# Performance work log

Hardware: AMD Instinct MI355X
Metric: run time of the kernel (lower is better)

Reference implementation:

```python
import jax, jax.numpy as jnp
import numpy as np

L, H, E, V = 8, 16, 1024, 32000   # n_layer, n_head, n_embd, vocab_size
B, T = 4, 1024                      # batch, block_size
HS = E // H                         # head_size = 64


def _ln(x, g, b, eps=1e-5):
    m = jnp.mean(x, axis=-1, keepdims=True)
    v = jnp.mean((x - m) ** 2, axis=-1, keepdims=True)
    return (x - m) / jnp.sqrt(v + eps) * g + b


def setup_inputs() -> dict:
    key = jax.random.key(0)
    ks = jax.random.split(key, 21)
    s = 0.02
    n = lambda k, shp: (jax.random.normal(k, shp, dtype=jnp.float32) * s)
    return {
        'idx': jax.random.randint(ks[0], (B, T), 0, V),
        'tok_emb': n(ks[1], (V, E)),
        'pos_emb': n(ks[2], (T, E)),
        'ln1_g': jnp.ones((L, E), jnp.float32),
        'ln1_b': jnp.zeros((L, E), jnp.float32),
        'Wq': n(ks[3], (L, E, E)),
        'Wk': n(ks[4], (L, E, E)),
        'Wv': n(ks[5], (L, E, E)),
        'Wo': n(ks[6], (L, E, E)),
        'bo': jnp.zeros((L, E), jnp.float32),
        'ln2_g': jnp.ones((L, E), jnp.float32),
        'ln2_b': jnp.zeros((L, E), jnp.float32),
        'W1': n(ks[7], (L, E, 4 * E)),
        'b1': jnp.zeros((L, 4 * E), jnp.float32),
        'W2': n(ks[8], (L, 4 * E, E)),
        'b2': jnp.zeros((L, E), jnp.float32),
        'lnf_g': jnp.ones((E,), jnp.float32),
        'lnf_b': jnp.zeros((E,), jnp.float32),
        'Wlm': n(ks[9], (E, V)),
        'blm': jnp.zeros((V,), jnp.float32),
    }


def reference(idx, tok_emb, pos_emb, ln1_g, ln1_b, Wq, Wk, Wv, Wo, bo,
              ln2_g, ln2_b, W1, b1, W2, b2, lnf_g, lnf_b, Wlm, blm):
    x = tok_emb[idx] + pos_emb[:T]               # [B, T, E]
    scale = E ** -0.5                            # NOTE: source scales by C=n_embd, not head_size
    mask = jnp.tril(jnp.ones((T, T), dtype=bool))
    for l in range(L):
        h = _ln(x, ln1_g[l], ln1_b[l])
        q = (h @ Wq[l]).reshape(B, T, H, HS).transpose(0, 2, 1, 3)   # [B,H,T,hs]
        k = (h @ Wk[l]).reshape(B, T, H, HS).transpose(0, 2, 1, 3)
        v = (h @ Wv[l]).reshape(B, T, H, HS).transpose(0, 2, 1, 3)
        att = jnp.einsum('bhqd,bhkd->bhqk', q, k) * scale
        att = jnp.where(mask, att, -jnp.inf)
        att = jax.nn.softmax(att, axis=-1)
        o = jnp.einsum('bhqk,bhkd->bhqd', att, v)
        o = o.transpose(0, 2, 1, 3).reshape(B, T, E)                 # concat heads
        x = x + o @ Wo[l] + bo[l]
        h2 = _ln(x, ln2_g[l], ln2_b[l])
        x = x + jax.nn.relu(h2 @ W1[l] + b1[l]) @ W2[l] + b2[l]
    x = _ln(x, lnf_g, lnf_b)
    return x @ Wlm + blm                          # logits [B, T, V]
```

## Files before the change

kernel.cpp:

```cpp
#include <hip/hip_runtime.h>
#include <math.h>

#define L_ 8
#define H_ 16
#define E_ 1024
#define V_ 32000
#define B_ 4
#define T_ 1024
#define HS_ 64
#define M_ 4096
#define QKVS_ 3072

typedef __attribute__((ext_vector_type(8))) short short8;
typedef __attribute__((ext_vector_type(4))) float f32x4;

__device__ __forceinline__ unsigned short f2bf(float f) {
  unsigned int u = __builtin_bit_cast(unsigned int, f);
  u += 0x7fffu + ((u >> 16) & 1u);
  return (unsigned short)(u >> 16);
}

__global__ __launch_bounds__(256) void k_embed(
    const int* __restrict__ idx, const float* __restrict__ tok,
    const float* __restrict__ pos, float* __restrict__ x) {
  int bt = blockIdx.x;
  int t  = bt & (T_ - 1);
  int token = idx[bt];
  const float4* te = (const float4*)(tok + (size_t)token * E_);
  const float4* pe = (const float4*)(pos + (size_t)t * E_);
  float4* xo = (float4*)(x + (size_t)bt * E_);
  int i = threadIdx.x;
  float4 a = te[i], b = pe[i];
  xo[i] = make_float4(a.x + b.x, a.y + b.y, a.z + b.z, a.w + b.w);
}

__global__ __launch_bounds__(256) void k_wt(
    const float* __restrict__ W, unsigned short* __restrict__ WT,
    int K, int N, size_t ss, size_t ds) {
  __shared__ unsigned short t[64][66];
  const float* Ws = W + (size_t)blockIdx.z * ss;
  unsigned short* Wd = WT + (size_t)blockIdx.z * ds;
  int n0 = blockIdx.x * 64, k0 = blockIdx.y * 64;
  int tid = threadIdx.x;
  int c = tid & 63, r4 = tid >> 6;
  #pragma unroll
  for (int i = 0; i < 16; ++i) {
    int kr = i * 4 + r4;
    t[kr][c] = f2bf(Ws[(size_t)(k0 + kr) * N + n0 + c]);
  }
  __syncthreads();
  #pragma unroll
  for (int i = 0; i < 16; ++i) {
    int nr = i * 4 + r4;
    Wd[(size_t)(n0 + nr) * K + k0 + c] = t[c][nr];
  }
}

__device__ __forceinline__ float blk_sum256(float v, float* red) {
  #pragma unroll
  for (int o = 1; o < 64; o <<= 1) v += __shfl_xor(v, o);
  int wid = threadIdx.x >> 6, lane = threadIdx.x & 63;
  if (lane == 0) red[wid] = v;
  __syncthreads();
  v = red[0] + red[1] + red[2] + red[3];
  __syncthreads();
  return v;
}

__global__ __launch_bounds__(256) void k_ln_bf(
    const float* __restrict__ X, const float* __restrict__ g,
    const float* __restrict__ b, unsigned short* __restrict__ Y) {
  __shared__ float red[4];
  int row = blockIdx.x;
  int i = threadIdx.x;
  float4 xv = ((const float4*)(X + (size_t)row * E_))[i];
  float s = xv.x + xv.y + xv.z + xv.w;
  s = blk_sum256(s, red);
  float mean = s * (1.0f / E_);
  float dx = xv.x - mean, dy = xv.y - mean, dz = xv.z - mean, dw = xv.w - mean;
  float vs = dx*dx + dy*dy + dz*dz + dw*dw;
  vs = blk_sum256(vs, red);
  float rstd = rsqrtf(vs * (1.0f / E_) + 1e-5f);
  float4 gv = ((const float4*)g)[i];
  float4 bv = ((const float4*)b)[i];
  ushort4 o;
  o.x = f2bf(dx * rstd * gv.x + bv.x);
  o.y = f2bf(dy * rstd * gv.y + bv.y);
  o.z = f2bf(dz * rstd * gv.z + bv.z);
  o.w = f2bf(dw * rstd * gv.w + bv.w);
  ((ushort4*)(Y + (size_t)row * E_))[i] = o;
}

template<int BN, int OT, bool RELU, bool RES>
__global__ __launch_bounds__(256) void k_gemm_tn(
    const unsigned short* __restrict__ A, const unsigned short* __restrict__ BT,
    const float* __restrict__ bias, const float* __restrict__ R,
    void* __restrict__ Cout, int M, int N, int K) {
  constexpr int NF = BN / 32;
  __shared__ __attribute__((aligned(16))) unsigned short As[128 * 64];
  __shared__ __attribute__((aligned(16))) unsigned short Bs[BN * 64];
  int tid = threadIdx.x;
  int lane = tid & 63, w = tid >> 6;
  int lr = lane & 15, lq = lane >> 4;
  int m0 = blockIdx.x * 128, n0 = blockIdx.y * BN;
  int wr = (w >> 1) * 64, wc = (w & 1) * (BN / 2);

  int srow = w * 8 + (lane >> 3);
  int skoff = ((lane & 7) ^ (lane >> 3)) * 8;
  const unsigned short* a0 = A + (size_t)(m0 + srow) * K + skoff;
  const unsigned short* b0 = BT + (size_t)(n0 + srow) * K + skoff;

  f32x4 acc[4][NF] = {};

  for (int k0 = 0; k0 < K; k0 += 64) {
    __syncthreads();
    #pragma unroll
    for (int j = 0; j < 4; ++j)
      __builtin_amdgcn_global_load_lds(
          (const __attribute__((address_space(1))) void*)(a0 + (size_t)(j * 32) * K + k0),
          (__attribute__((address_space(3))) void*)(As + j * 2048 + w * 512), 16, 0, 0);
    #pragma unroll
    for (int j = 0; j < NF; ++j)
      __builtin_amdgcn_global_load_lds(
          (const __attribute__((address_space(1))) void*)(b0 + (size_t)(j * 32) * K + k0),
          (__attribute__((address_space(3))) void*)(Bs + j * 2048 + w * 512), 16, 0, 0);
    __syncthreads();
    short8 af[4][2], bf[NF][2];
    #pragma unroll
    for (int m = 0; m < 4; ++m)
      #pragma unroll
      for (int ks = 0; ks < 2; ++ks)
        af[m][ks] = *(const short8*)&As[(wr + m * 16 + lr) * 64 + (((ks * 4 + lq) ^ (lr & 7)) << 3)];
    #pragma unroll
    for (int n = 0; n < NF; ++n)
      #pragma unroll
      for (int ks = 0; ks < 2; ++ks)
        bf[n][ks] = *(const short8*)&Bs[(wc + n * 16 + lr) * 64 + (((ks * 4 + lq) ^ (lr & 7)) << 3)];
    #pragma unroll
    for (int ks = 0; ks < 2; ++ks)
      #pragma unroll
      for (int m = 0; m < 4; ++m)
        #pragma unroll
        for (int n = 0; n < NF; ++n)
          acc[m][n] = __builtin_amdgcn_mfma_f32_16x16x32_bf16(af[m][ks], bf[n][ks], acc[m][n], 0, 0, 0);
  }

  #pragma unroll
  for (int m = 0; m < 4; ++m) {
    #pragma unroll
    for (int n = 0; n < NF; ++n) {
      int col = n0 + wc + n * 16 + lr;
      float bv = bias ? bias[col] : 0.0f;
      #pragma unroll
      for (int i = 0; i < 4; ++i) {
        size_t row = (size_t)(m0 + wr + m * 16 + lq * 4 + i);
        float v = acc[m][n][i] + bv;
        if (RELU) v = fmaxf(v, 0.0f);
        if (RES)  v += R[row * N + col];
        if (OT == 0) ((float*)Cout)[row * N + col] = v;
        else ((unsigned short*)Cout)[row * N + col] = f2bf(v);
      }
    }
  }
}

template<int OT, bool RELU, bool RES>
__global__ __launch_bounds__(256) void k_gemm_bf(
    const unsigned short* __restrict__ A, const float* __restrict__ W,
    const float* __restrict__ bias, const float* __restrict__ R,
    void* __restrict__ Cout, int M, int N, int K) {
  __shared__ unsigned short As[128][40];
  __shared__ unsigned short Bs[128][40];
  int tid = threadIdx.x;
  int lane = tid & 63, wid = tid >> 6;
  int m0 = blockIdx.x * 128, n0 = blockIdx.y * 128;
  int wr = (wid >> 1) * 64, wc = (wid & 1) * 64;
  f32x4 acc[4][4] = {};
  int a_row = tid >> 1, a_koff = (tid & 1) * 16;
  int b_nb = tid & 31, b_kb = (tid >> 5) * 4;
  int lr = lane & 15, lq = lane >> 4;
  for (int k0 = 0; k0 < K; k0 += 32) {
    const unsigned short* ap = A + (size_t)(m0 + a_row) * K + k0 + a_koff;
    uint4 av0 = *(const uint4*)ap;
    uint4 av1 = *(const uint4*)(ap + 8);
    float wv[4][4];
    #pragma unroll
    for (int dk = 0; dk < 4; ++dk) {
      const float* wrow = W + (size_t)(k0 + b_kb + dk) * N + n0 + b_nb;
      #pragma unroll
      for (int j = 0; j < 4; ++j) wv[j][dk] = wrow[32 * j];
    }
    __syncthreads();
    *(uint4*)&As[a_row][a_koff]     = av0;
    *(uint4*)&As[a_row][a_koff + 8] = av1;
    #pragma unroll
    for (int j = 0; j < 4; ++j) {
      ushort4 pk;
      pk.x = f2bf(wv[j][0]); pk.y = f2bf(wv[j][1]);
      pk.z = f2bf(wv[j][2]); pk.w = f2bf(wv[j][3]);
      *(ushort4*)&Bs[b_nb + 32 * j][b_kb] = pk;
    }
    __syncthreads();
    short8 af[4], bf[4];
    #pragma unroll
    for (int m = 0; m < 4; ++m) af[m] = *(const short8*)&As[wr + m * 16 + lr][lq * 8];
    #pragma unroll
    for (int n = 0; n < 4; ++n) bf[n] = *(const short8*)&Bs[wc + n * 16 + lr][lq * 8];
    #pragma unroll
    for (int m = 0; m < 4; ++m)
      #pragma unroll
      for (int n = 0; n < 4; ++n)
        acc[m][n] = __builtin_amdgcn_mfma_f32_16x16x32_bf16(af[m], bf[n], acc[m][n], 0, 0, 0);
  }
  #pragma unroll
  for (int m = 0; m < 4; ++m) {
    #pragma unroll
    for (int n = 0; n < 4; ++n) {
      int col = n0 + wc + n * 16 + lr;
      float bv = bias ? bias[col] : 0.0f;
      #pragma unroll
      for (int i = 0; i < 4; ++i) {
        size_t row = (size_t)(m0 + wr + m * 16 + lq * 4 + i);
        float v = acc[m][n][i] + bv;
        if (RELU) v = fmaxf(v, 0.0f);
        if (RES)  v += R[row * N + col];
        if (OT == 0) ((float*)Cout)[row * N + col] = v;
        else ((unsigned short*)Cout)[row * N + col] = f2bf(v);
      }
    }
  }
}

__global__ __launch_bounds__(256) void k_fattn(
    const unsigned short* __restrict__ QKV, unsigned short* __restrict__ O) {
  __shared__ unsigned short Ks[64][72];
  __shared__ unsigned short Vs[64][74];
  __shared__ unsigned short Pl[4][32][72];
  int tid = threadIdx.x;
  int lane = tid & 63, wid = tid >> 6;
  int lr = lane & 15, lq = lane >> 4;
  int qt = blockIdx.x, bh = blockIdx.y;
  int b = bh >> 4, h = bh & 15;
  size_t base = ((size_t)b * T_) * QKVS_ + h * HS_;
  int q0w = qt * 128 + wid * 32;

  short8 qf[2][2];
  #pragma unroll
  for (int g = 0; g < 2; ++g)
    #pragma unroll
    for (int s = 0; s < 2; ++s)
      qf[g][s] = *(const short8*)(QKV + base + (size_t)(q0w + g * 16 + lr) * QKVS_ + s * 32 + lq * 8);

  f32x4 o_acc[2][4] = {};
  float mrun[2][4], lrun[2][4];
  #pragma unroll
  for (int g = 0; g < 2; ++g)
    #pragma unroll
    for (int i = 0; i < 4; ++i) { mrun[g][i] = -1e30f; lrun[g][i] = 0.0f; }
  const float sc = 0.03125f * 1.44269504f;
  int r = tid >> 2, cc = (tid & 3) * 16;
  int ntiles = 2 * qt + 2;

  for (int t = 0; t < ntiles; ++t) {
    __syncthreads();
    const unsigned short* kp = QKV + base + 1024 + (size_t)(t * 64 + r) * QKVS_ + cc;
    const unsigned short* vp = kp + 1024;
    uint4 k0v = *(const uint4*)kp, k1v = *(const uint4*)(kp + 8);
    uint4 v0v = *(const uint4*)vp, v1v = *(const uint4*)(vp + 8);
    *(uint4*)&Ks[r][cc] = k0v;
    *(uint4*)&Ks[r][cc + 8] = k1v;
    unsigned short vt[16];
    *(uint4*)&vt[0] = v0v; *(uint4*)&vt[8] = v1v;
    #pragma unroll
    for (int j = 0; j < 16; ++j) Vs[cc + j][r] = vt[j];
    __syncthreads();

    f32x4 sa[2][4] = {};
    #pragma unroll
    for (int nt = 0; nt < 4; ++nt)
      #pragma unroll
      for (int s = 0; s < 2; ++s) {
        short8 kf = *(const short8*)&Ks[nt * 16 + lr][s * 32 + lq * 8];
        sa[0][nt] = __builtin_amdgcn_mfma_f32_16x16x32_bf16(qf[0][s], kf, sa[0][nt], 0, 0, 0);
        sa[1][nt] = __builtin_amdgcn_mfma_f32_16x16x32_bf16(qf[1][s], kf, sa[1][nt], 0, 0, 0);
      }

    bool diag = (t >= 2 * qt);
    float p[2][4][4];
    #pragma unroll
    for (int g = 0; g < 2; ++g)
      #pragma unroll
      for (int nt = 0; nt < 4; ++nt)
        #pragma unroll
        for (int i = 0; i < 4; ++i) {
          float v = sa[g][nt][i] * sc;
          if (diag && (t * 64 + nt * 16 + lr > q0w + g * 16 + lq * 4 + i)) v = -1e30f;
          p[g][nt][i] = v;
        }
    #pragma unroll
    for (int g = 0; g < 2; ++g)
      #pragma unroll
      for (int i = 0; i < 4; ++i) {
        float v = fmaxf(fmaxf(p[g][0][i], p[g][1][i]), fmaxf(p[g][2][i], p[g][3][i]));
        #pragma unroll
        for (int o = 1; o < 16; o <<= 1) v = fmaxf(v, __shfl_xor(v, o));
        float mn = fmaxf(mrun[g][i], v);
        float corr = __builtin_amdgcn_exp2f(mrun[g][i] - mn);
        mrun[g][i] = mn;
        float ps = 0.0f;
        #pragma unroll
        for (int nt = 0; nt < 4; ++nt) {
          float pe = __builtin_amdgcn_exp2f(p[g][nt][i] - mn);
          p[g][nt][i] = pe;
          ps += pe;
        }
        lrun[g][i] = lrun[g][i] * corr + ps;
        #pragma unroll
        for (int dn = 0; dn < 4; ++dn) o_acc[g][dn][i] *= corr;
      }
    #pragma unroll
    for (int g = 0; g < 2; ++g)
      #pragma unroll
      for (int nt = 0; nt < 4; ++nt)
        #pragma unroll
        for (int i = 0; i < 4; ++i)
          Pl[wid][g * 16 + lq * 4 + i][nt * 16 + lr] = f2bf(p[g][nt][i]);
    __syncthreads();

    #pragma unroll
    for (int s = 0; s < 2; ++s) {
      short8 pa0 = *(const short8*)&Pl[wid][lr][s * 32 + lq * 8];
      short8 pa1 = *(const short8*)&Pl[wid][16 + lr][s * 32 + lq * 8];
      #pragma unroll
      for (int dn = 0; dn < 4; ++dn) {
        short8 vf = *(const short8*)&Vs[dn * 16 + lr][s * 32 + lq * 8];
        o_acc[0][dn] = __builtin_amdgcn_mfma_f32_16x16x32_bf16(pa0, vf, o_acc[0][dn], 0, 0, 0);
        o_acc[1][dn] = __builtin_amdgcn_mfma_f32_16x16x32_bf16(pa1, vf, o_acc[1][dn], 0, 0, 0);
      }
    }
  }

  #pragma unroll
  for (int g = 0; g < 2; ++g)
    #pragma unroll
    for (int i = 0; i < 4; ++i) {
      float v = lrun[g][i];
      #pragma unroll
      for (int o = 1; o < 16; o <<= 1) v += __shfl_xor(v, o);
      lrun[g][i] = 1.0f / v;
    }
  #pragma unroll
  for (int g = 0; g < 2; ++g)
    #pragma unroll
    for (int dn = 0; dn < 4; ++dn)
      #pragma unroll
      for (int i = 0; i < 4; ++i) {
        size_t row = (size_t)(b * T_) + q0w + g * 16 + lq * 4 + i;
        O[row * E_ + h * HS_ + dn * 16 + lr] = f2bf(o_acc[g][dn][i] * lrun[g][i]);
      }
}

extern "C" void kernel_launch(void* const* d_in, const int* in_sizes, int n_in,
                              void* d_out, int out_size, void* d_ws, size_t ws_size,
                              hipStream_t stream) {
  const int*   idx  = (const int*)d_in[0];
  const float* tok  = (const float*)d_in[1];
  const float* pos  = (const float*)d_in[2];
  const float* ln1g = (const float*)d_in[3];
  const float* ln1b = (const float*)d_in[4];
  const float* Wq   = (const float*)d_in[5];
  const float* Wk   = (const float*)d_in[6];
  const float* Wv   = (const float*)d_in[7];
  const float* Wo   = (const float*)d_in[8];
  const float* bo   = (const float*)d_in[9];
  const float* ln2g = (const float*)d_in[10];
  const float* ln2b = (const float*)d_in[11];
  const float* W1   = (const float*)d_in[12];
  const float* b1   = (const float*)d_in[13];
  const float* W2   = (const float*)d_in[14];
  const float* b2   = (const float*)d_in[15];
  const float* lnfg = (const float*)d_in[16];
  const float* lnfb = (const float*)d_in[17];
  const float* Wlm  = (const float*)d_in[18];
  const float* blm  = (const float*)d_in[19];

  char* scr = (char*)d_out;
  const size_t MB = 1024 * 1024;
  float*          xf    = (float*)(scr);
  unsigned short* qkvb  = (unsigned short*)(scr + 16 * MB);
  unsigned short* ob    = (unsigned short*)(scr + 40 * MB);
  unsigned short* mh    = (unsigned short*)(scr + 48 * MB);
  unsigned short* wqkvT = (unsigned short*)(scr + 80 * MB);
  unsigned short* woT   = (unsigned short*)(scr + 128 * MB);
  unsigned short* w1T   = (unsigned short*)(scr + 144 * MB);
  unsigned short* w2T   = (unsigned short*)(scr + 208 * MB);
  unsigned short* hb    = (unsigned short*)d_ws;
  unsigned short* wlmT  = (unsigned short*)((char*)d_ws + 8 * MB);
  const size_t EE = (size_t)E_ * E_;
  bool lm_fast = ws_size >= 8 * MB + (size_t)V_ * E_ * 2 + 1024;

  k_embed<<<M_, 256, 0, stream>>>(idx, tok, pos, xf);

  k_wt<<<dim3(16, 16, L_), 256, 0, stream>>>(Wq, wqkvT,          E_, E_, EE, 3 * EE);
  k_wt<<<dim3(16, 16, L_), 256, 0, stream>>>(Wk, wqkvT + EE,     E_, E_, EE, 3 * EE);
  k_wt<<<dim3(16, 16, L_), 256, 0, stream>>>(Wv, wqkvT + 2 * EE, E_, E_, EE, 3 * EE);
  k_wt<<<dim3(16, 16, L_), 256, 0, stream>>>(Wo, woT,            E_, E_, EE, EE);
  k_wt<<<dim3(64, 16, L_), 256, 0, stream>>>(W1, w1T, E_, 4 * E_, 4 * EE, 4 * EE);
  k_wt<<<dim3(16, 64, L_), 256, 0, stream>>>(W2, w2T, 4 * E_, E_, 4 * EE, 4 * EE);
  if (lm_fast)
    k_wt<<<dim3(V_ / 64, 16, 1), 256, 0, stream>>>(Wlm, wlmT, E_, V_, 0, 0);

  for (int l = 0; l < L_; ++l) {
    k_ln_bf<<<M_, 256, 0, stream>>>(xf, ln1g + l * E_, ln1b + l * E_, hb);
    k_gemm_tn<128, 1, false, false><<<dim3(32, 24), 256, 0, stream>>>(
        hb, wqkvT + (size_t)l * 3 * EE, nullptr, nullptr, qkvb, M_, QKVS_, E_);
    k_fattn<<<dim3(T_ / 128, B_ * H_), 256, 0, stream>>>(qkvb, ob);
    k_gemm_tn<64, 0, false, true><<<dim3(32, 16), 256, 0, stream>>>(
        ob, woT + (size_t)l * EE, bo + l * E_, xf, xf, M_, E_, E_);
    k_ln_bf<<<M_, 256, 0, stream>>>(xf, ln2g + l * E_, ln2b + l * E_, hb);
    k_gemm_tn<128, 1, true, false><<<dim3(32, 32), 256, 0, stream>>>(
        hb, w1T + (size_t)l * 4 * EE, b1 + (size_t)l * 4 * E_, nullptr, mh, M_, 4 * E_, E_);
    k_gemm_tn<64, 0, false, true><<<dim3(32, 16), 256, 0, stream>>>(
        mh, w2T + (size_t)l * 4 * EE, b2 + l * E_, xf, xf, M_, E_, 4 * E_);
  }
  k_ln_bf<<<M_, 256, 0, stream>>>(xf, lnfg, lnfb, hb);
  if (lm_fast)
    k_gemm_tn<128, 0, false, false><<<dim3(32, V_ / 128), 256, 0, stream>>>(
        hb, wlmT, blm, nullptr, (float*)d_out, M_, V_, E_);
  else
    k_gemm_bf<0, false, false><<<dim3(32, V_ / 128), 256, 0, stream>>>(
        hb, Wlm, blm, nullptr, (float*)d_out, M_, V_, E_);
}
```

Measured before the change: 2.706 ms.

## Add 256x256 double-buffered GEMM with direct-to-LDS loads for QKV, FFN1, LM head

Introduces a new 512-thread GEMM kernel with 256x256 output tiles and a double-buffered LDS pipeline fed by global_load_lds. It interleaves MFMA phases with staged loads, raises wave priority around the MFMAs, and remaps workgroups so consecutive tiles land on the same XCD. It replaces the 128-tile kernel for the QKV, W1 and LM-head GEMMs, aiming for more data reuse per tile and better overlap of loads with compute. The cost is higher register and LDS pressure, and fewer workgroups for the smaller GEMMs, which can hurt occupancy and wave balance.

Result: faster. 2.644 ms (-2.3%).

```diff
diff --git a/kernel.cpp b/kernel.cpp
--- a/kernel.cpp
+++ b/kernel.cpp
@@ -89,6 +89,119 @@
   o.z = f2bf(dz * rstd * gv.z + bv.z);
   o.w = f2bf(dw * rstd * gv.w + bv.w);
   ((ushort4*)(Y + (size_t)row * E_))[i] = o;
+}
+
+#define BUFE 16384
+
+#define GLDS(src, dst) __builtin_amdgcn_global_load_lds( \
+    (const __attribute__((address_space(1))) void*)(src), \
+    (__attribute__((address_space(3))) void*)(dst), 16, 0, 0)
+
+#define BAR() do { asm volatile("" ::: "memory"); __builtin_amdgcn_s_barrier(); \
+                   asm volatile("" ::: "memory"); } while (0)
+
+template<int OT, bool RELU>
+__global__ __launch_bounds__(512, 2) void k_gemm_256(
+    const unsigned short* __restrict__ A, const unsigned short* __restrict__ BT,
+    const float* __restrict__ bias, void* __restrict__ Cout, int N, int K) {
+  __shared__ __attribute__((aligned(16))) unsigned short As[2 * BUFE];
+  __shared__ __attribute__((aligned(16))) unsigned short Bs[2 * BUFE];
+  int tid = threadIdx.x;
+  int lane = tid & 63, w = tid >> 6;
+  int lr = lane & 15, lq = (lane >> 4) & 3;
+  int wm = w >> 2, wn = w & 3;
+
+  int nwg = gridDim.x, orig = blockIdx.x;
+  int qq = nwg >> 3, rr = nwg & 7;
+  int xcd = orig & 7, lid = orig >> 3;
+  int wg = (xcd < rr ? xcd * (qq + 1) : rr * (qq + 1) + (xcd - rr) * qq) + lid;
+  int m0 = (wg & 15) * 256;
+  int n0 = (wg >> 4) * 256;
+
+  int srow = w * 8 + (lane >> 3);
+  int skoff = ((lane & 7) ^ (lane >> 3)) * 8;
+  const unsigned short* aS = A + (size_t)(m0 + srow) * K + skoff;
+  const unsigned short* bS = BT + (size_t)(n0 + srow) * K + skoff;
+
+#define STG_A(boff, half, tt) { \
+  GLDS(aS + (size_t)((half) * 128) * K + (tt) * 64,        &As[(boff) + (((half) * 128) << 6) + (w << 9)]); \
+  GLDS(aS + (size_t)((half) * 128 + 64) * K + (tt) * 64,   &As[(boff) + (((half) * 128 + 64) << 6) + (w << 9)]); }
+#define STG_B(boff, half, tt) { \
+  GLDS(bS + (size_t)((half) * 128) * K + (tt) * 64,        &Bs[(boff) + (((half) * 128) << 6) + (w << 9)]); \
+  GLDS(bS + (size_t)((half) * 128 + 64) * K + (tt) * 64,   &Bs[(boff) + (((half) * 128 + 64) << 6) + (w << 9)]); }
+#define LDA_(dst, mh, ks) { _Pragma("unroll") for (int m_ = 0; m_ < 4; ++m_) \
+  dst[m_] = *(const short8*)&As[so + ((wm * 128 + (mh) * 64 + m_ * 16 + lr) << 6) + ((((ks) * 4 + lq) ^ (lr & 7)) << 3)]; }
+#define LDB_(dst, ks) { _Pragma("unroll") for (int n_ = 0; n_ < 4; ++n_) \
+  dst[n_] = *(const short8*)&Bs[so + ((wn * 64 + n_ * 16 + lr) << 6) + ((((ks) * 4 + lq) ^ (lr & 7)) << 3)]; }
+#define MMA(afr, mofs) do { __builtin_amdgcn_s_setprio(1); \
+  _Pragma("unroll") for (int m_ = 0; m_ < 4; ++m_) { \
+    _Pragma("unroll") for (int n_ = 0; n_ < 4; ++n_) \
+      acc[(mofs) + m_][n_] = __builtin_amdgcn_mfma_f32_16x16x32_bf16(afr[m_], bfr[n_], acc[(mofs) + m_][n_], 0, 0, 0); } \
+  __builtin_amdgcn_s_setprio(0); } while (0)
+
+  f32x4 acc[8][4] = {};
+  const int NT = K >> 6;
+
+  STG_A(0, 0, 0); STG_A(0, 1, 0); STG_B(0, 0, 0); STG_B(0, 1, 0);
+  if (NT > 1) {
+    STG_B(BUFE, 0, 1);
+    asm volatile("s_waitcnt vmcnt(2)" ::: "memory");
+  } else {
+    asm volatile("s_waitcnt vmcnt(0)" ::: "memory");
+  }
+  BAR();
+
+  for (int t = 0; t < NT; ++t) {
+    const int so = (t & 1) * BUFE;
+    const int nbuf = ((t + 1) & 1) * BUFE;
+    short8 af0[4], af1[4], bfr[4];
+    LDA_(af0, 0, 0);
+    LDB_(bfr, 0);
+    if (t + 1 < NT) { STG_B(nbuf, 1, t + 1); }
+    BAR();
+    MMA(af0, 0);
+    BAR();
+    LDA_(af1, 1, 0);
+    if (t + 1 < NT) { STG_A(nbuf, 0, t + 1); }
+    BAR();
+    MMA(af1, 4);
+    BAR();
+    LDA_(af0, 0, 1);
+    LDB_(bfr, 1);
+    if (t + 1 < NT) { STG_A(nbuf, 1, t + 1); }
+    BAR();
+    MMA(af0, 0);
+    BAR();
+    LDA_(af1, 1, 1);
+    if (t + 2 < NT) { STG_B(so, 0, t + 2); }
+    BAR();
+    MMA(af1, 4);
+    if (t + 2 < NT) { asm volatile("s_waitcnt vmcnt(2)" ::: "memory"); }
+    else            { asm volatile("s_waitcnt vmcnt(0)" ::: "memory"); }
+    BAR();
+  }
+
+  #pragma unroll
+  for (int m = 0; m < 8; ++m) {
+    #pragma unroll
+    for (int n = 0; n < 4; ++n) {
+      int col = n0 + wn * 64 + n * 16 + lr;
+      float bv = bias ? bias[col] : 0.0f;
+      #pragma unroll
+      for (int i = 0; i < 4; ++i) {
+        size_t row = (size_t)(m0 + wm * 128 + m * 16 + lq * 4 + i);
+        float v = acc[m][n][i] + bv;
+        if (RELU) v = fmaxf(v, 0.0f);
+        if (OT == 0) ((float*)Cout)[row * N + col] = v;
+        else ((unsigned short*)Cout)[row * N + col] = f2bf(v);
+      }
+    }
+  }
+#undef STG_A
+#undef STG_B
+#undef LDA_
+#undef LDB_
+#undef MMA
 }
 
 template<int BN, int OT, bool RELU, bool RES>
@@ -412,21 +525,21 @@
 
   for (int l = 0; l < L_; ++l) {
     k_ln_bf<<<M_, 256, 0, stream>>>(xf, ln1g + l * E_, ln1b + l * E_, hb);
-    k_gemm_tn<128, 1, false, false><<<dim3(32, 24), 256, 0, stream>>>(
-        hb, wqkvT + (size_t)l * 3 * EE, nullptr, nullptr, qkvb, M_, QKVS_, E_);
+    k_gemm_256<1, false><<<16 * (QKVS_ / 256), 512, 0, stream>>>(
+        hb, wqkvT + (size_t)l * 3 * EE, nullptr, qkvb, QKVS_, E_);
     k_fattn<<<dim3(T_ / 128, B_ * H_), 256, 0, stream>>>(qkvb, ob);
     k_gemm_tn<64, 0, false, true><<<dim3(32, 16), 256, 0, stream>>>(
         ob, woT + (size_t)l * EE, bo + l * E_, xf, xf, M_, E_, E_);
     k_ln_bf<<<M_, 256, 0, stream>>>(xf, ln2g + l * E_, ln2b + l * E_, hb);
-    k_gemm_tn<128, 1, true, false><<<dim3(32, 32), 256, 0, stream>>>(
-        hb, w1T + (size_t)l * 4 * EE, b1 + (size_t)l * 4 * E_, nullptr, mh, M_, 4 * E_, E_);
+    k_gemm_256<1, true><<<16 * (4 * E_ / 256), 512, 0, stream>>>(
+        hb, w1T + (size_t)l * 4 * EE, b1 + (size_t)l * 4 * E_, mh, 4 * E_, E_);
     k_gemm_tn<64, 0, false, true><<<dim3(32, 16), 256, 0, stream>>>(
         mh, w2T + (size_t)l * 4 * EE, b2 + l * E_, xf, xf, M_, E_, 4 * E_);
   }
   k_ln_bf<<<M_, 256, 0, stream>>>(xf, lnfg, lnfb, hb);
   if (lm_fast)
-    k_gemm_tn<128, 0, false, false><<<dim3(32, V_ / 128), 256, 0, stream>>>(
-        hb, wlmT, blm, nullptr, (float*)d_out, M_, V_, E_);
+    k_gemm_256<0, false><<<16 * (V_ / 256), 512, 0, stream>>>(
+        hb, wlmT, blm, (float*)d_out, V_, E_);
   else
     k_gemm_bf<0, false, false><<<dim3(32, V_ / 128), 256, 0, stream>>>(
         hb, Wlm, blm, nullptr, (float*)d_out, M_, V_, E_);
```
